# Performance work log

Hardware: AMD Instinct MI355X
Metric: run time of the kernel (lower is better)

## Reference

```python
import jax, jax.numpy as jnp
import numpy as np
from jax import lax

MAX_ID = 32        # instance ids in the 3d grid are 0..MAX_ID-1
NUM_CLASSES = 13   # semantic labels 0..12 (wall=10, floor=11)
RADIUS = 3
GRID = (256, 256, 256)
SURFACE_THRESH = 1.5
WALL_CLASS, WALL_ID = 10, 1
FLOOR_CLASS, FLOOR_ID = 11, 2
THINGS_START = 2

# offsets in the same lexicographic order as nn_search's triple loop: range(-R, R)
_r = np.arange(-RADIUS, RADIUS)
OFFSETS = np.stack(np.meshgrid(_r, _r, _r, indexing='ij'), -1).reshape(-1, 3).astype(np.int32)


def setup_inputs() -> dict:
    key = jax.random.key(0)
    k1, k2, k3, k4 = jax.random.split(key, 4)
    geometry = jax.random.normal(k1, GRID, dtype=jnp.float32)            # TSDF-like grid
    instances = jax.random.randint(k2, GRID, 0, MAX_ID, dtype=jnp.int32)
    semantics = jax.random.randint(k3, GRID, 0, NUM_CLASSES, dtype=jnp.int32)
    ids2d = jax.random.randint(k4, (16,), 0, MAX_ID, dtype=jnp.int32)    # instances2d['locations'][0]
    return {'geometry': geometry, 'instances': instances, 'semantics': semantics, 'ids2d': ids2d}


def _postprocess(geometry, instances, semantics, ids2d):
    inst_flat = instances.ravel()
    ids2d_p1 = ids2d + 1

    # filter_instances: keep only 3d ids present in (2d instance ids + 1)
    sel_mask = jnp.isin(instances, ids2d_p1)                 # filtered = instances * sel_mask
    zero_present = jnp.any(~sel_mask).astype(jnp.int32)      # does unique(filtered) contain 0?

    # per-id presence; panoptic id = (index of id in unique(filtered)) + THINGS_START
    hist = jnp.bincount(inst_flat, length=MAX_ID + 1)        # voxel count per id
    in2d = jnp.isin(jnp.arange(1, MAX_ID + 1), ids2d_p1)
    present = in2d & (hist[1:] > 0)                          # for ids 1..MAX_ID
    rank = jnp.cumsum(present.astype(jnp.int32))             # 1-based rank among present ids
    pano_ids = jnp.where(present, rank - 1 + zero_present + THINGS_START, 0)
    pano_lut = jnp.zeros(MAX_ID + 1, jnp.int32).at[1:].set(pano_ids)
    panoptic = pano_lut[instances]                           # assign per instances==id masks

    # majority semantic label per instance, excluding {0, wall, floor}
    counts = jnp.zeros((MAX_ID + 1, NUM_CLASSES), jnp.int32).at[inst_flat, semantics.ravel()].add(1)
    counts = counts.at[:, jnp.array([0, WALL_CLASS, FLOOR_CLASS])].set(-1)
    sel_label = jnp.argmax(counts[1:], axis=1).astype(jnp.int32)

    # stuff overrides
    panoptic = jnp.where(semantics == WALL_CLASS, WALL_ID, panoptic)
    panoptic = jnp.where(semantics == FLOOR_CLASS, FLOOR_ID, panoptic)

    surface = jnp.abs(geometry) <= SURFACE_THRESH
    unassigned = surface & (panoptic == 0)
    grid0 = panoptic                                          # panoptic_instances_copy

    def body(carry, off):
        label, found = carry
        shifted = jnp.roll(grid0, shift=-off, axis=(0, 1, 2))  # shifted[p] = grid0[p + off]
        new = (shifted > 0) & ~found
        return (jnp.where(new, shifted, label), found | new), None

    init = (jnp.zeros(GRID, jnp.int32), jnp.zeros(GRID, dtype=bool))
    (nn_label, _), _ = lax.scan(body, init, jnp.asarray(OFFSETS))
    panoptic = jnp.where(unassigned, nn_label, grid0)

    # panoptic id -> semantic label LUT (disjoint ids, order-independent)
    sem_lut = (jnp.zeros(MAX_ID + THINGS_START + 1, jnp.int32)
               .at[WALL_ID].set(WALL_CLASS).at[FLOOR_ID].set(FLOOR_CLASS))
    sem_lut = sem_lut.at[pano_ids].set(jnp.where(present, sel_label, 0))
    panoptic_semantics = sem_lut[panoptic]
    return panoptic, panoptic_semantics


def reference(geometry, instances, semantics, ids2d):
    return jax.jit(_postprocess)(geometry, instances, semantics, ids2d)
```

## Files before the change

kernel.cpp:

```cpp
#include <hip/hip_runtime.h>
#include <stdint.h>

#define GRID_N (256*256*256)
#define MAXID 32
#define NCLS 13
#define NBINS ((MAXID+1)*NCLS)
#define PREP_BLOCKS 4096


__device__ __forceinline__ uint8_t keyb(int a, int b, float g) {
    int k = (b == 11) ? 33 : ((b == 10) ? 32 : a);
    return (uint8_t)(k | ((fabsf(g) <= 1.5f) ? 64 : 0));
}

__global__ __launch_bounds__(256) void k_prep(const float* __restrict__ geo,
                                              const int* __restrict__ inst,
                                              const int* __restrict__ sem,
                                              const int* __restrict__ ids2d, int n2d,
                                              int* __restrict__ counts8,
                                              unsigned int* __restrict__ seenArr,
                                              uint8_t* __restrict__ key) {
    __shared__ int sh[4][NBINS];
    __shared__ unsigned int wseen[4];
    int t = threadIdx.x;
    for (int i = t; i < 4 * NBINS; i += 256) ((int*)sh)[i] = 0;
    __syncthreads();
    int* myh = sh[t >> 6];

    uint64_t m = 0;
    for (int k = 0; k < n2d; ++k) m |= 1ull << (ids2d[k] + 1);
    const unsigned int eligC = 0x13FE;

    unsigned int seen = 0;
    const int stride = PREP_BLOCKS * 256;
    const int4*   i4 = (const int4*)inst;
    const int4*   s4 = (const int4*)sem;
    const float4* g4 = (const float4*)geo;
    uchar4*       k4 = (uchar4*)key;

    int idx = blockIdx.x * 256 + t;
    #pragma unroll
    for (int it = 0; it < 4; ++it, idx += stride) {
        int4 a = i4[idx];
        int4 b = s4[idx];
        float4 g = g4[idx];
        uchar4 kk;
        kk.x = keyb(a.x, b.x, g.x);
        kk.y = keyb(a.y, b.y, g.y);
        kk.z = keyb(a.z, b.z, g.z);
        kk.w = keyb(a.w, b.w, g.w);
        k4[idx] = kk;
        seen |= (1u << a.x) | (1u << a.y) | (1u << a.z) | (1u << a.w);
        if (((unsigned)(m >> a.x) & (eligC >> b.x)) & 1)
            atomicAdd(&myh[a.x * NCLS + b.x], 1);
        if (((unsigned)(m >> a.y) & (eligC >> b.y)) & 1)
            atomicAdd(&myh[a.y * NCLS + b.y], 1);
        if (((unsigned)(m >> a.z) & (eligC >> b.z)) & 1)
            atomicAdd(&myh[a.z * NCLS + b.z], 1);
        if (((unsigned)(m >> a.w) & (eligC >> b.w)) & 1)
            atomicAdd(&myh[a.w * NCLS + b.w], 1);
    }

    #pragma unroll
    for (int o = 32; o; o >>= 1) seen |= (unsigned int)__shfl_xor((int)seen, o);
    if ((t & 63) == 0) wseen[t >> 6] = seen;
    __syncthreads();
    if (t == 0)
        seenArr[blockIdx.x] = wseen[0] | wseen[1] | wseen[2] | wseen[3];

    int* dst = counts8 + (blockIdx.x & 7) * NBINS;
    for (int i = t; i < NBINS; i += 256) {
        int v = sh[0][i] + sh[1][i] + sh[2][i] + sh[3][i];
        if (v) atomicAdd(&dst[i], v);
    }
}

__global__ __launch_bounds__(512) void k_luts(const int* __restrict__ counts8,
                                              const unsigned int* __restrict__ seenArr,
                                              const int* __restrict__ ids2d, int n2d,
                                              int* __restrict__ glut) {
    __shared__ int shc[NBINS];
    __shared__ int sem_s[35];
    __shared__ unsigned int wseen[8];
    int t = threadIdx.x;

    unsigned int s = 0;
    #pragma unroll
    for (int i = 0; i < 8; ++i) s |= seenArr[t + i * 512];
    #pragma unroll
    for (int o = 32; o; o >>= 1) s |= (unsigned int)__shfl_xor((int)s, o);
    if ((t & 63) == 0) wseen[t >> 6] = s;

    if (t < NBINS) {
        int acc = 0;
        #pragma unroll
        for (int c = 0; c < 8; ++c) acc += counts8[c * NBINS + t];
        shc[t] = acc;
    }
    __syncthreads();
    if (t < 64) {
        unsigned int seen = wseen[0] | wseen[1] | wseen[2] | wseen[3]
                          | wseen[4] | wseen[5] | wseen[6] | wseen[7];
        uint64_t m = 0;
        for (int k = 0; k < n2d; ++k) m |= 1ull << (ids2d[k] + 1);

        int in2d_t = (t <= MAXID) ? (int)((m >> t) & 1) : 0;
        int seen_t = (t < 32) ? (int)((seen >> t) & 1) : 0;
        int sel_t = 0;
        if (t <= MAXID) {
            int best = -2;
            for (int c = 0; c < NCLS; ++c) {
                int v = (c == 0 || c == 10 || c == 11) ? -1 : shc[t * NCLS + c];
                if (v > best) { best = v; sel_t = c; }
            }
        }
        int zero_present = ((seen & ~(unsigned int)m) != 0u) ? 1 : 0;
        int pres = (t >= 1 && in2d_t && seen_t) ? 1 : 0;
        unsigned long long pm = __ballot(pres);
        int rank_below = __popcll(pm & ((1ULL << t) - 1ULL));
        int pano_id = pres ? (rank_below + zero_present + 2) : 0;

        if (t < 35) sem_s[t] = (t == 1) ? 10 : ((t == 2) ? 11 : 0);
        if (pres) sem_s[pano_id] = sel_t;

        if (t < 32) glut[t] = (t == 0) ? 0 : pano_id;
        if (t == 32) glut[32] = 1;
        if (t == 33) glut[33] = 2;
        if (t < 35) glut[34 + t] = sem_s[t];
    }
}

#define TX 8
#define TY 8
#define HR 13
#define NROWS (HR*HR)
#define ROWDW 66
#define NDW (NROWS*ROWDW)

__global__ __launch_bounds__(512) void k_nn(const uint8_t* __restrict__ key,
                                            const int* __restrict__ glut,
                                            int* __restrict__ out_pano,
                                            int* __restrict__ out_sem) {
    __shared__ uint32_t shg[NDW];
    __shared__ int lut[128];
    __shared__ int slut[MAXID + 3];

    int t = threadIdx.x;
    if (t < 128) {
        int base = ((t & 63) <= 33) ? glut[t & 63] : 0;
        lut[t] = base | ((t & 64) << 1);
    } else if (t >= 128 && t < 128 + MAXID + 3) {
        slut[t - 128] = glut[34 + (t - 128)];
    }
    __syncthreads();

    int x0 = blockIdx.x * TX;
    int y0 = blockIdx.y * TY;

    const uint32_t* key32 = (const uint32_t*)key;
    for (int idx = t; idx < NDW; idx += 512) {
        int row = idx / ROWDW;
        int k = idx - row * ROWDW;
        int ix = row / HR;
        int iy = row - ix * HR;
        int gx = (x0 + ix - 3) & 255;
        int gy = (y0 + iy - 3) & 255;
        uint32_t w = key32[(gx << 14) | (gy << 6) | ((k - 1) & 63)];
        shg[idx] = (uint32_t)lut[w & 127]
                 | ((uint32_t)lut[(w >> 8) & 127] << 8)
                 | ((uint32_t)lut[(w >> 16) & 127] << 16)
                 | ((uint32_t)lut[(w >> 24) & 127] << 24);
    }
    __syncthreads();

    int zg = t & 63;
    int ty = t >> 6;
    int gy = y0 + ty;
    const uint64_t M6 = 0x00007F7F7F7F7F7FULL;

    for (int x = 0; x < TX; ++x) {
        int gx = x0 + x;
        int r0 = (x + 3) * HR + (ty + 3);
        uint32_t cw = shg[r0 * ROWDW + zg + 1];
        int4 pano, semv;
        int pv[4];
        #pragma unroll
        for (int b = 0; b < 4; ++b) {
            int v = (cw >> (8 * b)) & 255;
            int p = v & 127;
            if (p == 0 && (v & 128)) {
                int z = 4 * zg + b;
                int label = 0;
                int j0 = z + 1;
                int a0 = j0 >> 2, off = j0 & 3;
                for (int dxi = 0; dxi < 6 && !label; ++dxi) {
                    int rb = ((x + dxi) * HR + ty) * ROWDW + a0;
                    for (int dyi = 0; dyi < 6; ++dyi) {
                        int a = rb + dyi * ROWDW;
                        uint32_t d0 = shg[a], d1 = shg[a + 1], d2 = shg[a + 2];
                        uint64_t lo = (uint64_t)d0 | ((uint64_t)d1 << 32);
                        uint64_t win = lo >> (off * 8);
                        if (off) win |= (uint64_t)d2 << (64 - off * 8);
                        uint64_t mask = win & M6;
                        if (mask) {
                            int bb = __ffsll((long long)mask) - 1;
                            label = (int)((win >> (bb & 56)) & 0x7f);
                            break;
                        }
                    }
                }
                p = label;
            }
            pv[b] = p;
        }
        pano.x = pv[0]; pano.y = pv[1]; pano.z = pv[2]; pano.w = pv[3];
        semv.x = slut[pv[0]]; semv.y = slut[pv[1]]; semv.z = slut[pv[2]]; semv.w = slut[pv[3]];
        int oi = (gx << 14) | (gy << 6) | zg;
        ((int4*)out_pano)[oi] = pano;
        ((int4*)out_sem)[oi] = semv;
    }
}

extern "C" void kernel_launch(void* const* d_in, const int* in_sizes, int n_in,
                              void* d_out, int out_size, void* d_ws, size_t ws_size,
                              hipStream_t stream) {
    const float* geo   = (const float*)d_in[0];
    const int*   inst  = (const int*)d_in[1];
    const int*   sem   = (const int*)d_in[2];
    const int*   ids2d = (const int*)d_in[3];
    const int    n2d   = in_sizes[3];

    char* ws = (char*)d_ws;
    int* counts8           = (int*)(ws);
    unsigned int* seenArr  = (unsigned int*)(ws + 16384);
    int* glut              = (int*)(ws + 32768);
    uint8_t* key           = (uint8_t*)(ws + 49152);

    int* out_pano = (int*)d_out;
    int* out_sem  = out_pano + GRID_N;

    hipMemsetAsync(counts8, 0, 16384, stream);
    k_prep<<<PREP_BLOCKS, 256, 0, stream>>>(geo, inst, sem, ids2d, n2d,
                                            counts8, seenArr, key);
    k_luts<<<1, 512, 0, stream>>>(counts8, seenArr, ids2d, n2d, glut);
    dim3 g(32, 32);
    k_nn<<<g, 512, 0, stream>>>(key, glut, out_pano, out_sem);
}
```

Baseline: 305.6 us.

## Split prep into streaming pack kernel and histogram kernel over packed keys

The fused prep kernel is split in two. The first kernel streams geometry, instance and semantic grids and packs each voxel into a 16-bit key (id, class, surface bit), using the output buffer as scratch. The second kernel reads those compact keys, builds the per-instance class histogram with shared atomics, collects the seen-id bitmask and writes the 8-bit key used by the neighbour kernel. The block count doubles and partial-count copies go from 8 to 16. The aim is to keep the bandwidth-bound pass free of atomic stalls, at the cost of an extra kernel launch and an extra 32 MB write plus read of the 16-bit intermediate.

```diff
diff --git a/kernel.cpp b/kernel.cpp
--- a/kernel.cpp
+++ b/kernel.cpp
@@ -5,21 +5,43 @@
 #define MAXID 32
 #define NCLS 13
 #define NBINS ((MAXID+1)*NCLS)
-#define PREP_BLOCKS 4096
-
-
-__device__ __forceinline__ uint8_t keyb(int a, int b, float g) {
-    int k = (b == 11) ? 33 : ((b == 10) ? 32 : a);
-    return (uint8_t)(k | ((fabsf(g) <= 1.5f) ? 64 : 0));
-}
-
-__global__ __launch_bounds__(256) void k_prep(const float* __restrict__ geo,
-                                              const int* __restrict__ inst,
-                                              const int* __restrict__ sem,
-                                              const int* __restrict__ ids2d, int n2d,
-                                              int* __restrict__ counts8,
-                                              unsigned int* __restrict__ seenArr,
-                                              uint8_t* __restrict__ key) {
+#define PREP_BLOCKS 8192
+
+
+__global__ __launch_bounds__(256) void k_prepA(const float* __restrict__ geo,
+                                               const int* __restrict__ inst,
+                                               const int* __restrict__ sem,
+                                               uint16_t* __restrict__ key16) {
+    int t = blockIdx.x * 256 + threadIdx.x;
+    const int stride = PREP_BLOCKS * 256;
+    const int4*   i4 = (const int4*)inst;
+    const int4*   s4 = (const int4*)sem;
+    const float4* g4 = (const float4*)geo;
+    ushort4*      k4 = (ushort4*)key16;
+
+    int idx0 = t, idx1 = t + stride;
+    int4 a0 = i4[idx0], a1 = i4[idx1];
+    int4 b0 = s4[idx0], b1 = s4[idx1];
+    float4 g0 = g4[idx0], g1 = g4[idx1];
+
+    ushort4 k0, k1;
+    k0.x = (uint16_t)(a0.x | (b0.x << 5) | ((fabsf(g0.x) <= 1.5f) ? 512 : 0));
+    k0.y = (uint16_t)(a0.y | (b0.y << 5) | ((fabsf(g0.y) <= 1.5f) ? 512 : 0));
+    k0.z = (uint16_t)(a0.z | (b0.z << 5) | ((fabsf(g0.z) <= 1.5f) ? 512 : 0));
+    k0.w = (uint16_t)(a0.w | (b0.w << 5) | ((fabsf(g0.w) <= 1.5f) ? 512 : 0));
+    k1.x = (uint16_t)(a1.x | (b1.x << 5) | ((fabsf(g1.x) <= 1.5f) ? 512 : 0));
+    k1.y = (uint16_t)(a1.y | (b1.y << 5) | ((fabsf(g1.y) <= 1.5f) ? 512 : 0));
+    k1.z = (uint16_t)(a1.z | (b1.z << 5) | ((fabsf(g1.z) <= 1.5f) ? 512 : 0));
+    k1.w = (uint16_t)(a1.w | (b1.w << 5) | ((fabsf(g1.w) <= 1.5f) ? 512 : 0));
+    k4[idx0] = k0;
+    k4[idx1] = k1;
+}
+
+__global__ __launch_bounds__(256) void k_prepB(const uint16_t* __restrict__ key16,
+                                               const int* __restrict__ ids2d, int n2d,
+                                               int* __restrict__ counts16,
+                                               unsigned int* __restrict__ seenArr,
+                                               uint8_t* __restrict__ key8) {
     __shared__ int sh[4][NBINS];
     __shared__ unsigned int wseen[4];
     int t = threadIdx.x;
@@ -31,51 +53,40 @@
     for (int k = 0; k < n2d; ++k) m |= 1ull << (ids2d[k] + 1);
     const unsigned int eligC = 0x13FE;
 
+    int idx = blockIdx.x * 256 + t;
+    uint4 w = ((const uint4*)key16)[idx];
     unsigned int seen = 0;
-    const int stride = PREP_BLOCKS * 256;
-    const int4*   i4 = (const int4*)inst;
-    const int4*   s4 = (const int4*)sem;
-    const float4* g4 = (const float4*)geo;
-    uchar4*       k4 = (uchar4*)key;
-
-    int idx = blockIdx.x * 256 + t;
-    #pragma unroll
-    for (int it = 0; it < 4; ++it, idx += stride) {
-        int4 a = i4[idx];
-        int4 b = s4[idx];
-        float4 g = g4[idx];
-        uchar4 kk;
-        kk.x = keyb(a.x, b.x, g.x);
-        kk.y = keyb(a.y, b.y, g.y);
-        kk.z = keyb(a.z, b.z, g.z);
-        kk.w = keyb(a.w, b.w, g.w);
-        k4[idx] = kk;
-        seen |= (1u << a.x) | (1u << a.y) | (1u << a.z) | (1u << a.w);
-        if (((unsigned)(m >> a.x) & (eligC >> b.x)) & 1)
-            atomicAdd(&myh[a.x * NCLS + b.x], 1);
-        if (((unsigned)(m >> a.y) & (eligC >> b.y)) & 1)
-            atomicAdd(&myh[a.y * NCLS + b.y], 1);
-        if (((unsigned)(m >> a.z) & (eligC >> b.z)) & 1)
-            atomicAdd(&myh[a.z * NCLS + b.z], 1);
-        if (((unsigned)(m >> a.w) & (eligC >> b.w)) & 1)
-            atomicAdd(&myh[a.w * NCLS + b.w], 1);
-    }
-
-    #pragma unroll
-    for (int o = 32; o; o >>= 1) seen |= (unsigned int)__shfl_xor((int)seen, o);
+    uint32_t out_lo = 0, out_hi = 0;
+    uint32_t ws_[4] = {w.x, w.y, w.z, w.w};
+    #pragma unroll
+    for (int j = 0; j < 8; ++j) {
+        uint32_t v = (ws_[j >> 1] >> ((j & 1) * 16)) & 0xFFFF;
+        int id = v & 31, cls = (v >> 5) & 15, surf = (v >> 9) & 1;
+        seen |= 1u << id;
+        int kid = (cls == 11) ? 33 : ((cls == 10) ? 32 : id);
+        uint32_t kb = (uint32_t)(kid | (surf << 6));
+        if (j < 4) out_lo |= kb << (8 * j); else out_hi |= kb << (8 * (j - 4));
+        if (((unsigned)(m >> id) & (eligC >> cls)) & 1)
+            atomicAdd(&myh[id * NCLS + cls], 1);
+    }
+    uint2 o; o.x = out_lo; o.y = out_hi;
+    ((uint2*)key8)[idx] = o;
+
+    #pragma unroll
+    for (int off = 32; off; off >>= 1) seen |= (unsigned int)__shfl_xor((int)seen, off);
     if ((t & 63) == 0) wseen[t >> 6] = seen;
     __syncthreads();
     if (t == 0)
         seenArr[blockIdx.x] = wseen[0] | wseen[1] | wseen[2] | wseen[3];
 
-    int* dst = counts8 + (blockIdx.x & 7) * NBINS;
+    int* dst = counts16 + (blockIdx.x & 15) * NBINS;
     for (int i = t; i < NBINS; i += 256) {
         int v = sh[0][i] + sh[1][i] + sh[2][i] + sh[3][i];
         if (v) atomicAdd(&dst[i], v);
     }
 }
 
-__global__ __launch_bounds__(512) void k_luts(const int* __restrict__ counts8,
+__global__ __launch_bounds__(512) void k_luts(const int* __restrict__ counts16,
                                               const unsigned int* __restrict__ seenArr,
                                               const int* __restrict__ ids2d, int n2d,
                                               int* __restrict__ glut) {
@@ -86,7 +97,7 @@
 
     unsigned int s = 0;
     #pragma unroll
-    for (int i = 0; i < 8; ++i) s |= seenArr[t + i * 512];
+    for (int i = 0; i < 16; ++i) s |= seenArr[t + i * 512];
     #pragma unroll
     for (int o = 32; o; o >>= 1) s |= (unsigned int)__shfl_xor((int)s, o);
     if ((t & 63) == 0) wseen[t >> 6] = s;
@@ -94,7 +105,7 @@
     if (t < NBINS) {
         int acc = 0;
         #pragma unroll
-        for (int c = 0; c < 8; ++c) acc += counts8[c * NBINS + t];
+        for (int c = 0; c < 16; ++c) acc += counts16[c * NBINS + t];
         shc[t] = acc;
     }
     __syncthreads();
@@ -231,18 +242,20 @@
     const int    n2d   = in_sizes[3];
 
     char* ws = (char*)d_ws;
-    int* counts8           = (int*)(ws);
-    unsigned int* seenArr  = (unsigned int*)(ws + 16384);
-    int* glut              = (int*)(ws + 32768);
-    uint8_t* key           = (uint8_t*)(ws + 49152);
+    int* counts16          = (int*)(ws);
+    unsigned int* seenArr  = (unsigned int*)(ws + 32768);
+    int* glut              = (int*)(ws + 65536);
+    uint8_t* key8          = (uint8_t*)(ws + 69632);
 
     int* out_pano = (int*)d_out;
     int* out_sem  = out_pano + GRID_N;
-
-    hipMemsetAsync(counts8, 0, 16384, stream);
-    k_prep<<<PREP_BLOCKS, 256, 0, stream>>>(geo, inst, sem, ids2d, n2d,
-                                            counts8, seenArr, key);
-    k_luts<<<1, 512, 0, stream>>>(counts8, seenArr, ids2d, n2d, glut);
+    uint16_t* key16 = (uint16_t*)d_out;
+
+    hipMemsetAsync(counts16, 0, 32768, stream);
+    k_prepA<<<PREP_BLOCKS, 256, 0, stream>>>(geo, inst, sem, key16);
+    k_prepB<<<PREP_BLOCKS, 256, 0, stream>>>(key16, ids2d, n2d,
+                                             counts16, seenArr, key8);
+    k_luts<<<1, 512, 0, stream>>>(counts16, seenArr, ids2d, n2d, glut);
     dim3 g(32, 32);
-    k_nn<<<g, 512, 0, stream>>>(key, glut, out_pano, out_sem);
-}
+    k_nn<<<g, 512, 0, stream>>>(key8, glut, out_pano, out_sem);
+}
```

Result: slower. 324.2 us (+6.1%).
